# Kernel tuning notes

Hardware: AMD Instinct MI355X
Metric: run time of the kernel (lower is better)

## Reference

```python
import jax, jax.numpy as jnp
import numpy as np

B, R, H, E = 256, 2048, 64, 20
LN_EPS = 1e-5


def setup_inputs() -> dict:
    key = jax.random.key(0)
    ks = jax.random.split(key, 16)
    s = 0.05  # small init scale for weights
    return {
        "query_relations": jax.random.randint(ks[0], (B,), 0, R),
        "edge_type": jax.random.randint(ks[1], (B, E), 0, R),
        "base_relation_reprs": jax.random.normal(ks[2], (B, R, H), dtype=jnp.float32),
        "init_noise": jax.random.normal(ks[3], (B, R, H), dtype=jnp.float32),
        "msg_W": jax.random.normal(ks[4], (2 * H, H), dtype=jnp.float32) * s,
        "msg_b": jnp.zeros((H,), dtype=jnp.float32),
        "upd_W": jax.random.normal(ks[5], (H, H), dtype=jnp.float32) * s,
        "upd_b": jnp.zeros((H,), dtype=jnp.float32),
        "ln_g": jnp.ones((H,), dtype=jnp.float32),
        "ln_b": jnp.zeros((H,), dtype=jnp.float32),
        "fus_W1": jax.random.normal(ks[6], (2 * H, H), dtype=jnp.float32) * s,
        "fus_b1": jnp.zeros((H,), dtype=jnp.float32),
        "fus_W2": jax.random.normal(ks[7], (H, H), dtype=jnp.float32) * s,
        "fus_b2": jnp.zeros((H,), dtype=jnp.float32),
        "gate_W": jax.random.normal(ks[8], (2 * H, 1), dtype=jnp.float32) * s,
        "gate_b": jnp.zeros((1,), dtype=jnp.float32),
    }


def reference(query_relations, edge_type, base_relation_reprs, init_noise,
              msg_W, msg_b, upd_W, upd_b, ln_g, ln_b,
              fus_W1, fus_b1, fus_W2, fus_b2, gate_W, gate_b):
    # --- SimplePromptEncoder (batched over the per-sample prompt graphs) ---
    # relation_embeddings = randn*0.1, query-relation row set to ones.  [B, R, H]
    is_query = (jnp.arange(R)[None, :] == query_relations[:, None])[..., None]
    rel_emb = jnp.where(is_query, jnp.float32(1.0), init_noise * jnp.float32(0.1))
    # head_embeds == tail_embeds == rel_emb[edge_type]  (gather)      [B, E, H]
    h = jnp.take_along_axis(rel_emb, edge_type[..., None], axis=1)
    msg = jax.nn.relu(jnp.concatenate([h, h], axis=-1) @ msg_W + msg_b)  # [B, E, H]
    # scatter_add over edge_type per sample                            [B, R, H]
    agg = jax.vmap(lambda m, t: jax.ops.segment_sum(m, t, num_segments=R))(msg, edge_type)
    # update_net: Linear + LayerNorm
    upd = agg @ upd_W + upd_b
    mu = jnp.mean(upd, axis=-1, keepdims=True)
    var = jnp.mean((upd - mu) ** 2, axis=-1, keepdims=True)
    prompt = (upd - mu) / jnp.sqrt(var + LN_EPS) * ln_g + ln_b  # [B, R, H]
    # --- fusion + gating ---
    combined = jnp.concatenate([base_relation_reprs, prompt], axis=-1)  # [B, R, 2H]
    fused = jax.nn.relu(combined @ fus_W1 + fus_b1) @ fus_W2 + fus_b2   # [B, R, H]
    gate = jax.nn.sigmoid(combined @ gate_W + gate_b)                    # [B, R, 1]
    return gate * fused + (1.0 - gate) * base_relation_reprs
```

## Files before the change

### kernel.cpp

```cpp
#include <hip/hip_runtime.h>

#define B 256
#define R 2048
#define H 64
#define E 20
#define LN_EPS 1e-5f

#define NB_EDGE 256
#define NB_MAIN 1024
#define TILES_PER_BLOCK 8

typedef float f32x4 __attribute__((ext_vector_type(4)));
typedef short s16x8 __attribute__((ext_vector_type(8)));

__device__ __forceinline__ unsigned short f2bf(float x){
  unsigned int u = __float_as_uint(x);
  u += 0x7fffu + ((u >> 16) & 1u);
  return (unsigned short)(u >> 16);
}

__device__ __forceinline__ float wave64_sum(float v){
  #pragma unroll
  for (int m = 1; m < 64; m <<= 1) v += __shfl_xor(v, m, 64);
  return v;
}

struct MainS {
  unsigned short lw1[H*72];
  unsigned short lw2[H*72];
  unsigned short lhid[4][16*72];
  float lc1[H];
  float lb2[H];
  float lgw[H];
  float lgz;
};
struct EdgeS {
  float wsum[H*H];
  float msgbuf[E][H];
  int   et[E];
};
union SMem { MainS m; EdgeS e; };

__global__ __launch_bounds__(256) void fused_kernel(
    const int* __restrict__ qrel, const int* __restrict__ etype,
    const float* __restrict__ base, const float* __restrict__ noise,
    const float* __restrict__ msg_W, const float* __restrict__ msg_b,
    const float* __restrict__ upd_W, const float* __restrict__ upd_b,
    const float* __restrict__ ln_g,  const float* __restrict__ ln_b,
    const float* __restrict__ fus_W1,const float* __restrict__ fus_b1,
    const float* __restrict__ fus_W2,const float* __restrict__ fus_b2,
    const float* __restrict__ gate_W,const float* __restrict__ gate_b,
    int* __restrict__ trows, float* __restrict__ tprompt,
    float* __restrict__ out)
{
  __shared__ SMem smem;
  int tid = threadIdx.x;
  int w = tid >> 6, ln = tid & 63;

  if (blockIdx.x < NB_EDGE) {
    EdgeS* S = &smem.e;
    int b = blockIdx.x;
    if (tid < E) S->et[tid] = etype[b*E + tid];
    for (int i = tid; i < H*H; i += 256)
      S->wsum[i] = msg_W[i] + msg_W[H*H + i];
    __syncthreads();
    int q = qrel[b];

    #pragma unroll
    for (int i = 0; i < E/4; ++i) {
      int e = w + i*4;
      int r = S->et[e];
      float hv = (r == q) ? 1.0f : noise[((size_t)b*R + r)*H + ln] * 0.1f;
      float acc = msg_b[ln];
      #pragma unroll 8
      for (int k = 0; k < H; ++k)
        acc += __shfl(hv, k, 64) * S->wsum[k*H + ln];
      S->msgbuf[e][ln] = fmaxf(acc, 0.f);
    }
    __syncthreads();

    #pragma unroll
    for (int i = 0; i < E/4; ++i) {
      int e = w + i*4;
      int r = S->et[e];
      bool first = true;
      for (int e2 = 0; e2 < e; ++e2) if (S->et[e2] == r) first = false;
      if (!first) { if (ln == 0) trows[b*E + e] = -1; continue; }
      float agg = 0.f;
      for (int e2 = e; e2 < E; ++e2)
        if (S->et[e2] == r) agg += S->msgbuf[e2][ln];
      float u = upd_b[ln];
      #pragma unroll 8
      for (int k = 0; k < H; ++k)
        u += __shfl(agg, k, 64) * upd_W[k*H + ln];
      float mu = wave64_sum(u) * (1.0f/H);
      float d  = u - mu;
      float var= wave64_sum(d*d) * (1.0f/H);
      float p  = d * rsqrtf(var + LN_EPS) * ln_g[ln] + ln_b[ln];
      tprompt[(b*E + e)*H + ln] = p;
      if (ln == 0) trows[b*E + e] = r;
    }
    return;
  }

  MainS* S = &smem.m;
  for (int i = tid; i < H*H; i += 256) {
    int k = i >> 6, n = i & 63;
    S->lw1[n*72 + k] = f2bf(fus_W1[i]);
    S->lw2[n*72 + k] = f2bf(fus_W2[i]);
  }
  if (tid < H) {
    S->lb2[tid] = fus_b2[tid];
    S->lgw[tid] = gate_W[tid];
  }
  if (tid < 64) {
    float u  = upd_b[tid];
    float mu = wave64_sum(u) * (1.0f/H);
    float d  = u - mu;
    float var= wave64_sum(d*d) * (1.0f/H);
    float p  = d * rsqrtf(var + LN_EPS) * ln_g[tid] + ln_b[tid];
    float acc = fus_b1[tid];
    #pragma unroll 8
    for (int k = 0; k < H; ++k)
      acc += __shfl(p, k, 64) * fus_W1[(H+k)*H + tid];
    S->lc1[tid] = acc;
    float gp = p * gate_W[H + tid];
    gp = wave64_sum(gp);
    if (tid == 0) S->lgz = gp + gate_b[0];
  }
  __syncthreads();

  int m = ln & 15, q = ln >> 4;
  float gz = S->lgz;
  int mb = blockIdx.x - NB_EDGE;

  for (int it = 0; it < TILES_PER_BLOCK; ++it) {
    int rowbase = (mb*TILES_PER_BLOCK + it)*64 + w*16;
    const float* arow = base + (size_t)(rowbase + m)*H;

    f32x4 a0 = *(const f32x4*)(arow + q*8);
    f32x4 a1 = *(const f32x4*)(arow + q*8 + 4);
    f32x4 a2 = *(const f32x4*)(arow + 32 + q*8);
    f32x4 a3 = *(const f32x4*)(arow + 32 + q*8 + 4);

    float gp = 0.f;
    #pragma unroll
    for (int j = 0; j < 4; ++j) {
      gp += a0[j]*S->lgw[q*8+j]    + a1[j]*S->lgw[q*8+4+j];
      gp += a2[j]*S->lgw[32+q*8+j] + a3[j]*S->lgw[32+q*8+4+j];
    }
    gp += __shfl_xor(gp, 16, 64);
    gp += __shfl_xor(gp, 32, 64);
    float g = 1.0f / (1.0f + __expf(-(gp + gz)));

    s16x8 A0, A1;
    #pragma unroll
    for (int j = 0; j < 4; ++j) {
      A0[j]   = (short)f2bf(a0[j]);
      A0[j+4] = (short)f2bf(a1[j]);
      A1[j]   = (short)f2bf(a2[j]);
      A1[j+4] = (short)f2bf(a3[j]);
    }

    f32x4 hacc[4];
    #pragma unroll
    for (int ct = 0; ct < 4; ++ct) {
      const s16x8 B0 = *(const s16x8*)&S->lw1[(ct*16 + m)*72 + q*8];
      const s16x8 B1 = *(const s16x8*)&S->lw1[(ct*16 + m)*72 + 32 + q*8];
      float c1v = S->lc1[ct*16 + m];
      f32x4 c = {c1v, c1v, c1v, c1v};
      c = __builtin_amdgcn_mfma_f32_16x16x32_bf16(A0, B0, c, 0, 0, 0);
      hacc[ct] = __builtin_amdgcn_mfma_f32_16x16x32_bf16(A1, B1, c, 0, 0, 0);
    }
    #pragma unroll
    for (int ct = 0; ct < 4; ++ct) {
      #pragma unroll
      for (int r = 0; r < 4; ++r) {
        float v = fmaxf(hacc[ct][r], 0.f);
        S->lhid[w][(q*4 + r)*72 + ct*16 + m] = f2bf(v);
      }
    }
    s16x8 HA0 = *(const s16x8*)&S->lhid[w][m*72 + q*8];
    s16x8 HA1 = *(const s16x8*)&S->lhid[w][m*72 + 32 + q*8];

    f32x4 facc[4];
    #pragma unroll
    for (int ct = 0; ct < 4; ++ct) {
      const s16x8 B0 = *(const s16x8*)&S->lw2[(ct*16 + m)*72 + q*8];
      const s16x8 B1 = *(const s16x8*)&S->lw2[(ct*16 + m)*72 + 32 + q*8];
      f32x4 c = *(const f32x4*)&S->lb2[ct*16 + q*4];
      c = __builtin_amdgcn_mfma_f32_16x16x32_bf16(B0, HA0, c, 0, 0, 0);
      facc[ct] = __builtin_amdgcn_mfma_f32_16x16x32_bf16(B1, HA1, c, 0, 0, 0);
    }

    const float* brow = base + (size_t)(rowbase + m)*H;
    float*       orow = out  + (size_t)(rowbase + m)*H;
    #pragma unroll
    for (int ct = 0; ct < 4; ++ct) {
      int col = ct*16 + q*4;
      f32x4 bv = *(const f32x4*)(brow + col);
      f32x4 o;
      #pragma unroll
      for (int j = 0; j < 4; ++j)
        o[j] = fmaf(g, facc[ct][j] - bv[j], bv[j]);
      *(f32x4*)(orow + col) = o;
    }
  }
}

__global__ __launch_bounds__(256) void fixup_kernel(
    const float* __restrict__ base,
    const float* __restrict__ fus_W1, const float* __restrict__ fus_b1,
    const float* __restrict__ fus_W2, const float* __restrict__ fus_b2,
    const float* __restrict__ gate_W, const float* __restrict__ gate_b,
    const int* __restrict__ trows, const float* __restrict__ tprompt,
    float* __restrict__ out)
{
  __shared__ float W1s[2*H*H];
  __shared__ float W2s[H*H];
  int b = blockIdx.x, tid = threadIdx.x, w = tid >> 6, ln = tid & 63;
  for (int i = tid; i < 2*H*H; i += 256) W1s[i] = fus_W1[i];
  for (int i = tid; i < H*H;   i += 256) W2s[i] = fus_W2[i];
  __syncthreads();
  float gb = gate_b[0];
  #pragma unroll
  for (int i = 0; i < E/4; ++i) {
    int e = w + i*4;
    int r = trows[b*E + e];
    if (r < 0) continue;
    float bv = base[((size_t)b*R + r)*H + ln];
    float pv = tprompt[(b*E + e)*H + ln];
    float acc = fus_b1[ln];
    #pragma unroll 8
    for (int k = 0; k < H; ++k)
      acc += __shfl(bv, k, 64)*W1s[k*H + ln] + __shfl(pv, k, 64)*W1s[(H+k)*H + ln];
    float h = fmaxf(acc, 0.f);
    float f = fus_b2[ln];
    #pragma unroll 8
    for (int k = 0; k < H; ++k)
      f += __shfl(h, k, 64)*W2s[k*H + ln];
    float gp = bv*gate_W[ln] + pv*gate_W[H + ln];
    gp = wave64_sum(gp);
    float g = 1.0f/(1.0f + __expf(-(gp + gb)));
    out[((size_t)b*R + r)*H + ln] = fmaf(g, f - bv, bv);
  }
}

extern "C" void kernel_launch(void* const* d_in, const int* in_sizes, int n_in,
                              void* d_out, int out_size, void* d_ws, size_t ws_size,
                              hipStream_t stream)
{
  const int*   qrel   = (const int*)d_in[0];
  const int*   etyp   = (const int*)d_in[1];
  const float* base   = (const float*)d_in[2];
  const float* noise  = (const float*)d_in[3];
  const float* msg_W  = (const float*)d_in[4];
  const float* msg_b  = (const float*)d_in[5];
  const float* upd_W  = (const float*)d_in[6];
  const float* upd_b  = (const float*)d_in[7];
  const float* ln_g   = (const float*)d_in[8];
  const float* ln_b   = (const float*)d_in[9];
  const float* fus_W1 = (const float*)d_in[10];
  const float* fus_b1 = (const float*)d_in[11];
  const float* fus_W2 = (const float*)d_in[12];
  const float* fus_b2 = (const float*)d_in[13];
  const float* gate_W = (const float*)d_in[14];
  const float* gate_b = (const float*)d_in[15];
  float* out = (float*)d_out;

  char* ws = (char*)d_ws;
  float* tprompt = (float*)ws;
  int*   trows   = (int*)(ws + (size_t)B*E*H*4);

  fused_kernel<<<NB_EDGE + NB_MAIN, 256, 0, stream>>>(
      qrel, etyp, base, noise, msg_W, msg_b, upd_W, upd_b, ln_g, ln_b,
      fus_W1, fus_b1, fus_W2, fus_b2, gate_W, gate_b,
      trows, tprompt, out);
  fixup_kernel<<<B, 256, 0, stream>>>(base, fus_W1, fus_b1, fus_W2, fus_b2,
                                      gate_W, gate_b, trows, tprompt, out);
}
```

Baseline: 358.7 us.

## Fold edge blocks into main blocks and prefetch next row tile

Removes the separate edge-processing blocks. The first 256 main blocks now do the per-sample edge/prompt work, hit a barrier, and then run their fusion tiles, so the grid shrinks to NB_MAIN blocks. The main loop software-prefetches the next tile's base rows into registers while computing the current tile. The second MFMA loop is merged with the output epilogue so fewer accumulators are live. The risk is load imbalance, since 256 blocks now carry extra serial edge work ahead of their main tiles, and the prefetch raises register pressure.

```diff
diff --git a/kernel.cpp b/kernel.cpp
--- a/kernel.cpp
+++ b/kernel.cpp
@@ -100,7 +100,7 @@
       tprompt[(b*E + e)*H + ln] = p;
       if (ln == 0) trows[b*E + e] = r;
     }
-    return;
+    __syncthreads();
   }
 
   MainS* S = &smem.m;
@@ -113,7 +113,7 @@
     S->lb2[tid] = fus_b2[tid];
     S->lgw[tid] = gate_W[tid];
   }
-  if (tid < 64) {
+  if (tid < 64 && w == 0) {
     float u  = upd_b[tid];
     float mu = wave64_sum(u) * (1.0f/H);
     float d  = u - mu;
@@ -132,16 +132,29 @@
 
   int m = ln & 15, q = ln >> 4;
   float gz = S->lgz;
-  int mb = blockIdx.x - NB_EDGE;
+  int mb = blockIdx.x;
+
+  f32x4 a0, a1, a2, a3;
+  {
+    int rowbase = (mb*TILES_PER_BLOCK)*64 + w*16;
+    const float* arow = base + (size_t)(rowbase + m)*H;
+    a0 = *(const f32x4*)(arow + q*8);
+    a1 = *(const f32x4*)(arow + q*8 + 4);
+    a2 = *(const f32x4*)(arow + 32 + q*8);
+    a3 = *(const f32x4*)(arow + 32 + q*8 + 4);
+  }
 
   for (int it = 0; it < TILES_PER_BLOCK; ++it) {
     int rowbase = (mb*TILES_PER_BLOCK + it)*64 + w*16;
-    const float* arow = base + (size_t)(rowbase + m)*H;
-
-    f32x4 a0 = *(const f32x4*)(arow + q*8);
-    f32x4 a1 = *(const f32x4*)(arow + q*8 + 4);
-    f32x4 a2 = *(const f32x4*)(arow + 32 + q*8);
-    f32x4 a3 = *(const f32x4*)(arow + 32 + q*8 + 4);
+
+    f32x4 n0, n1, n2, n3;
+    if (it + 1 < TILES_PER_BLOCK) {
+      const float* nrow = base + (size_t)(rowbase + 64 + m)*H;
+      n0 = *(const f32x4*)(nrow + q*8);
+      n1 = *(const f32x4*)(nrow + q*8 + 4);
+      n2 = *(const f32x4*)(nrow + 32 + q*8);
+      n3 = *(const f32x4*)(nrow + 32 + q*8 + 4);
+    }
 
     float gp = 0.f;
     #pragma unroll
@@ -183,28 +196,26 @@
     s16x8 HA0 = *(const s16x8*)&S->lhid[w][m*72 + q*8];
     s16x8 HA1 = *(const s16x8*)&S->lhid[w][m*72 + 32 + q*8];
 
-    f32x4 facc[4];
+    const float* brow = base + (size_t)(rowbase + m)*H;
+    float*       orow = out  + (size_t)(rowbase + m)*H;
     #pragma unroll
     for (int ct = 0; ct < 4; ++ct) {
       const s16x8 B0 = *(const s16x8*)&S->lw2[(ct*16 + m)*72 + q*8];
       const s16x8 B1 = *(const s16x8*)&S->lw2[(ct*16 + m)*72 + 32 + q*8];
       f32x4 c = *(const f32x4*)&S->lb2[ct*16 + q*4];
       c = __builtin_amdgcn_mfma_f32_16x16x32_bf16(B0, HA0, c, 0, 0, 0);
-      facc[ct] = __builtin_amdgcn_mfma_f32_16x16x32_bf16(B1, HA1, c, 0, 0, 0);
-    }
-
-    const float* brow = base + (size_t)(rowbase + m)*H;
-    float*       orow = out  + (size_t)(rowbase + m)*H;
-    #pragma unroll
-    for (int ct = 0; ct < 4; ++ct) {
+      f32x4 facc = __builtin_amdgcn_mfma_f32_16x16x32_bf16(B1, HA1, c, 0, 0, 0);
+
       int col = ct*16 + q*4;
       f32x4 bv = *(const f32x4*)(brow + col);
       f32x4 o;
       #pragma unroll
       for (int j = 0; j < 4; ++j)
-        o[j] = fmaf(g, facc[ct][j] - bv[j], bv[j]);
+        o[j] = fmaf(g, facc[j] - bv[j], bv[j]);
       *(f32x4*)(orow + col) = o;
     }
+
+    a0 = n0; a1 = n1; a2 = n2; a3 = n3;
   }
 }
 
@@ -272,7 +283,7 @@
   float* tprompt = (float*)ws;
   int*   trows   = (int*)(ws + (size_t)B*E*H*4);
 
-  fused_kernel<<<NB_EDGE + NB_MAIN, 256, 0, stream>>>(
+  fused_kernel<<<NB_MAIN, 256, 0, stream>>>(
       qrel, etyp, base, noise, msg_W, msg_b, upd_W, upd_b, ln_g, ln_b,
       fus_W1, fus_b1, fus_W2, fus_b2, gate_W, gate_b,
       trows, tprompt, out);
```

Result: slower. 378.9 us (+5.6%).
